# Kernel optimization log

Measured on AMD Instinct MI355X. Metric: run time of the kernel, lower is better.

## Reference

```python
import jax, jax.numpy as jnp
import numpy as np

LRELU_GAIN = 2.0 ** 0.5  # util.lrelu_gain (assumed sqrt(2))
EPS = 1e-8


def upsample2_bilinear_ac(x):
    # F.upsample_bilinear == bilinear with align_corners=True, scale 2
    B, C, H, W = x.shape
    def lerp_axis(t, n, axis):
        c = jnp.arange(2 * n, dtype=jnp.float32) * (n - 1) / (2 * n - 1)
        i0 = jnp.floor(c).astype(jnp.int32)
        i1 = jnp.minimum(i0 + 1, n - 1)
        f = c - i0.astype(jnp.float32)
        a = jnp.take(t, i0, axis=axis)
        b = jnp.take(t, i1, axis=axis)
        shape = [1] * t.ndim
        shape[axis] = 2 * n
        f = f.reshape(shape)
        return a * (1.0 - f) + b * f
    x = lerp_axis(x, H, 2)
    x = lerp_axis(x, W, 3)
    return x


def conv1x1(x, weight, bias, gain):
    # Conv2dNormalizedLR with kernel_size=1: he = gain/sqrt(in)
    cin = weight.shape[1]
    he = gain / float(cin) ** 0.5
    y = jnp.einsum('bihw,oi->bohw', x, weight[:, :, 0, 0] * he)
    return y + bias[None, :, None, None]


def mod_conv3x3(x, weight, style, gain):
    # weight: [Cin, Cout, 3, 3]; style: [B, Cin]
    cin, cout, k, _ = weight.shape
    he = gain / float(cin * k * k) ** 0.5
    wmod = style[:, :, None, None, None] * (weight * he)[None]  # [B,Cin,Cout,k,k]
    # demodulation: normalize over (in, kh, kw) per out channel
    d = jax.lax.rsqrt(jnp.sum(wmod * wmod, axis=(1, 3, 4), keepdims=True) + EPS)
    wmod = wmod * d
    # conv_transpose2d(stride=1, pad=1, k=3) == conv2d with transposed+flipped kernel, pad=1
    kern = jnp.flip(jnp.transpose(wmod, (0, 2, 1, 3, 4)), axis=(3, 4))  # [B,Cout,Cin,k,k]
    def one(xb, kb):
        return jax.lax.conv_general_dilated(
            xb[None], kb, (1, 1), ((1, 1), (1, 1)),
            dimension_numbers=('NCHW', 'OIHW', 'NCHW'))[0]
    y = jax.vmap(one)(x, kern)
    return y * gain


def noise_affine(noise, w_s, b_s, w_b, b_b):
    # Baff*: 1x1 conv from 1 channel, gain=1 -> he=1
    ys = noise * w_s[None, :, 0, None, 0, None][:, :, :, 0] if False else noise * w_s[:, 0, 0, 0][None, :, None, None] + b_s[None, :, None, None]
    yb = noise * w_b[:, 0, 0, 0][None, :, None, None] + b_b[None, :, None, None]
    return ys, yb


def block_forward(x, w, noise1, noise2, conv1_w, bias1, conv2_w, bias2,
                  Aaff1_w, Aaff1_b, Aaff2_w, Aaff2_b,
                  Baff1s_w, Baff1s_b, Baff1b_w, Baff1b_b,
                  Baff2s_w, Baff2s_b, Baff2b_w, Baff2b_b,
                  rgb_w, rgb_b):
    x = upsample2_bilinear_ac(x)
    style1 = conv1x1(w, Aaff1_w, Aaff1_b, 1.0)[:, :, 0, 0]  # [B, Cin]
    x = mod_conv3x3(x, conv1_w, style1, LRELU_GAIN)
    ys, yb = noise_affine(noise1, Baff1s_w, Baff1s_b, Baff1b_w, Baff1b_b)
    x = x * ys + yb + bias1
    x = jax.nn.leaky_relu(x, 0.2)
    style2 = conv1x1(w, Aaff2_w, Aaff2_b, 1.0)[:, :, 0, 0]
    x = mod_conv3x3(x, conv2_w, style2, LRELU_GAIN)
    ys, yb = noise_affine(noise2, Baff2s_w, Baff2s_b, Baff2b_w, Baff2b_b)
    x = x * ys + yb + bias2
    x = jax.nn.leaky_relu(x, 0.2)
    rgb = conv1x1(x, rgb_w, rgb_b, 0.03)
    return x, rgb


def setup_inputs() -> dict:
    key = jax.random.key(0)
    ks = jax.random.split(key, 20)
    B, Cin, Cout, Wd, H, W = 8, 512, 512, 512, 32, 32
    inp = {
        'x': jax.random.normal(ks[0], (B, Cin, H, W), jnp.float32),
        'w': jax.random.normal(ks[1], (B, Wd, 1, 1), jnp.float32),
        'noise1': jax.random.normal(ks[2], (B, 1, 2 * H, 2 * W), jnp.float32),
        'noise2': jax.random.normal(ks[3], (B, 1, 2 * H, 2 * W), jnp.float32),
        'conv1_w': jax.random.normal(ks[4], (Cin, Cout, 3, 3), jnp.float32),
        'bias1': jnp.zeros((1, Cout, 1, 1), jnp.float32),
        'conv2_w': jax.random.normal(ks[5], (Cout, Cout, 3, 3), jnp.float32),
        'bias2': jnp.zeros((1, Cout, 1, 1), jnp.float32),
        'Aaff1_w': jax.random.normal(ks[6], (Cin, Wd, 1, 1), jnp.float32),
        'Aaff1_b': jnp.zeros((Cin,), jnp.float32),
        'Aaff2_w': jax.random.normal(ks[7], (Cout, Wd, 1, 1), jnp.float32),
        'Aaff2_b': jnp.zeros((Cout,), jnp.float32),
        'Baff1s_w': jax.random.normal(ks[8], (Cout, 1, 1, 1), jnp.float32) * 0.1,
        'Baff1s_b': jnp.ones((Cout,), jnp.float32),
        'Baff1b_w': jax.random.normal(ks[9], (Cout, 1, 1, 1), jnp.float32) * 0.1,
        'Baff1b_b': jnp.zeros((Cout,), jnp.float32),
        'Baff2s_w': jax.random.normal(ks[10], (Cout, 1, 1, 1), jnp.float32) * 0.1,
        'Baff2s_b': jnp.ones((Cout,), jnp.float32),
        'Baff2b_w': jax.random.normal(ks[11], (Cout, 1, 1, 1), jnp.float32) * 0.1,
        'Baff2b_b': jnp.zeros((Cout,), jnp.float32),
        'rgb_w': jax.random.normal(ks[12], (3, Cout, 1, 1), jnp.float32),
        'rgb_b': jnp.zeros((3,), jnp.float32),
    }
    return inp


def reference(x, w, noise1, noise2, conv1_w, bias1, conv2_w, bias2,
              Aaff1_w, Aaff1_b, Aaff2_w, Aaff2_b,
              Baff1s_w, Baff1s_b, Baff1b_w, Baff1b_b,
              Baff2s_w, Baff2s_b, Baff2b_w, Baff2b_b,
              rgb_w, rgb_b):
    return block_forward(x, w, noise1, noise2, conv1_w, bias1, conv2_w, bias2,
                         Aaff1_w, Aaff1_b, Aaff2_w, Aaff2_b,
                         Baff1s_w, Baff1s_b, Baff1b_w, Baff1b_b,
                         Baff2s_w, Baff2s_b, Baff2b_w, Baff2b_b,
                         rgb_w, rgb_b)
```

## Files before the change

kernel.cpp:

```cpp
#include <hip/hip_runtime.h>
#include <hip/hip_bf16.h>

#define BB 8
#define CC 512
#define HO 64
#define HP 66
#define NPIX (BB*HO*HO)

typedef float f32x4 __attribute__((ext_vector_type(4)));
typedef __bf16 bf16x8 __attribute__((ext_vector_type(8)));
using bf16 = __hip_bfloat16;

__device__ __forceinline__ void gload16(const void* g, void* l) {
    __builtin_amdgcn_global_load_lds((const __attribute__((address_space(1))) void*)g,
                                     (__attribute__((address_space(3))) void*)l, 16, 0, 0);
}

__device__ __forceinline__ float waveRedSum(float v) {
    #pragma unroll
    for (int off = 32; off; off >>= 1) v += __shfl_down(v, off);
    return v;
}

__global__ void prep_weights(const float* __restrict__ Wsrc, float* __restrict__ S2ho,
                             bf16* __restrict__ keffT, float he) {
    int t = blockIdx.x * blockDim.x + threadIdx.x;
    int i = t & (CC-1), o = t >> 9;
    const float* wp = Wsrc + (i*CC + o)*9;
    float v[9]; float s2 = 0.f;
    #pragma unroll
    for (int k = 0; k < 9; ++k) { v[k] = wp[k] * he; s2 += v[k]*v[k]; }
    S2ho[o*CC + i] = s2;
    #pragma unroll
    for (int tp = 0; tp < 9; ++tp) keffT[(tp*CC + o)*CC + i] = (bf16)v[8 - tp];
}

__global__ void style_kernel(const float* __restrict__ w,
                             const float* __restrict__ A1, const float* __restrict__ A1b,
                             const float* __restrict__ A2, const float* __restrict__ A2b,
                             float* __restrict__ s1, float* __restrict__ s2) {
    int wid = (blockIdx.x * blockDim.x + threadIdx.x) >> 6;
    int lane = threadIdx.x & 63;
    int set = wid >= BB*CC; int rem = set ? wid - BB*CC : wid;
    int b = rem >> 9, i = rem & (CC-1);
    const float* A = set ? A2 : A1;
    const float* wb = w + b*CC;
    float sum = 0.f;
    for (int d = lane; d < CC; d += 64) sum += wb[d] * A[i*CC + d];
    sum = waveRedSum(sum);
    if (lane == 0) {
        float r = sum * 0.04419417382415922f + (set ? A2b : A1b)[i];
        (set ? s2 : s1)[b*CC + i] = r;
    }
}

__global__ void demod_kernel(const float* __restrict__ s1, const float* __restrict__ S21,
                             const float* __restrict__ s2, const float* __restrict__ S22,
                             float* __restrict__ dg1, float* __restrict__ dg2, float gain) {
    int wid = (blockIdx.x * blockDim.x + threadIdx.x) >> 6;
    int lane = threadIdx.x & 63;
    int set = wid >= BB*CC; int rem = set ? wid - BB*CC : wid;
    int b = rem >> 9, o = rem & (CC-1);
    const float* st = (set ? s2 : s1) + b*CC;
    const float* S2 = (set ? S22 : S21) + o*CC;
    float sum = 0.f;
    for (int i = lane; i < CC; i += 64) { float sv = st[i]; sum += sv*sv*S2[i]; }
    sum = waveRedSum(sum);
    if (lane == 0) (set ? dg2 : dg1)[b*CC + o] = gain * rsqrtf(sum + 1e-8f);
}

__global__ void upsample_mod(const float* __restrict__ x, const float* __restrict__ s1,
                             bf16* __restrict__ xs1) {
    __shared__ float usl[16][CC];
    int blk = blockIdx.x;
    int i = threadIdx.x;
    int b = blk >> 10, rem = blk & 1023, p = rem >> 4, q0 = (rem & 15) << 2;
    const float scale = 31.0f / 63.0f;
    float chf = p * scale; int h0 = (int)chf; float fh = chf - h0; int h1 = min(h0 + 1, 31);
    int wa = min(((int)(q0 * scale)) & ~3, 24);
    const float* xb = x + ((size_t)(b*CC + i) << 10);
    f32x4 r00 = *(const f32x4*)(xb + (h0 << 5) + wa);
    f32x4 r01 = *(const f32x4*)(xb + (h0 << 5) + wa + 4);
    f32x4 r10 = *(const f32x4*)(xb + (h1 << 5) + wa);
    f32x4 r11 = *(const f32x4*)(xb + (h1 << 5) + wa + 4);
    #pragma unroll
    for (int k = 0; k < 4; ++k) {
        usl[k][i] = r00[k]; usl[4 + k][i] = r01[k];
        usl[8 + k][i] = r10[k]; usl[12 + k][i] = r11[k];
    }
    float sv = s1[b*CC + i];
    #pragma unroll
    for (int dq = 0; dq < 4; ++dq) {
        int q = q0 + dq;
        float cwf = q * scale; int w0 = (int)cwf; float fw = cwf - w0;
        int i0 = w0 - wa, i1 = min(w0 + 1, 31) - wa;
        float v00 = usl[i0][i], v01 = usl[i1][i];
        float v10 = usl[8 + i0][i], v11 = usl[8 + i1][i];
        float va = v00*(1.f-fh) + v10*fh;
        float vb = v01*(1.f-fh) + v11*fh;
        float v  = (va*(1.f-fw) + vb*fw) * sv;
        xs1[(((b*HP) + p + 1)*HP + (q + 1))*CC + i] = (bf16)v;
    }
}

#define SB  __builtin_amdgcn_sched_barrier(0)
#define BAR __builtin_amdgcn_s_barrier()
#define VMC(n)  asm volatile("s_waitcnt vmcnt(" #n ")" ::: "memory")
#define LGKM(n) asm volatile("s_waitcnt lgkmcnt(" #n ")" ::: "memory")

#define STAGE_A(d, h, U) do { \
    gload16((U) + aThr + (h)*(HP*1024),                 ldsA + (d)*32768 + (h)*16384); \
    gload16((U) + aThr + (h)*(HP*1024) + 2*(HP*1024),   ldsA + (d)*32768 + (h)*16384 + 8192); \
} while (0)

#define STAGE_B(d, h, U) do { \
    gload16((U) + bThr + (h)*32768,                     ldsB + (d)*32768 + (h)*16384); \
    gload16((U) + bThr + (h)*32768 + 131072,            ldsB + (d)*32768 + (h)*16384 + 8192); \
} while (0)

#define LOAD_A(d, fh) do { \
    _Pragma("unroll") \
    for (int fmq = 0; fmq < 4; ++fmq) { \
        afr[fmq][0] = *(const bf16x8*)(aRd + (d)*32768 + (fh)*16384 + fmq*2048 + swz0); \
        afr[fmq][1] = *(const bf16x8*)(aRd + (d)*32768 + (fh)*16384 + fmq*2048 + swz1); \
    } } while (0)

#define LOAD_B(d, nh) do { \
    _Pragma("unroll") \
    for (int fnq = 0; fnq < 2; ++fnq) { \
        bfr[nh][fnq][0] = *(const bf16x8*)(bRd + (d)*32768 + (nh)*16384 + fnq*2048 + swz0); \
        bfr[nh][fnq][1] = *(const bf16x8*)(bRd + (d)*32768 + (nh)*16384 + fnq*2048 + swz1); \
    } } while (0)

#define QUAD(fh, nh) do { \
    __builtin_amdgcn_s_setprio(1); \
    _Pragma("unroll") \
    for (int kc = 0; kc < 2; ++kc) \
    { _Pragma("unroll") \
      for (int fmq = 0; fmq < 4; ++fmq) \
      { _Pragma("unroll") \
        for (int fnq = 0; fnq < 2; ++fnq) \
            acc[(fh)*4+fmq][(nh)*2+fnq] = __builtin_amdgcn_mfma_f32_16x16x32_bf16( \
                afr[fmq][kc], bfr[nh][fnq][kc], acc[(fh)*4+fmq][(nh)*2+fnq], 0, 0, 0); } } \
    __builtin_amdgcn_s_setprio(0); } while (0)

#define PHSTEP(cur, nxt, aN1, bN1, aN2, g1, g3) do { \
     \
    LOAD_A(cur, 0); \
    LOAD_B(cur, 0); \
    if (g1) STAGE_B(nxt, 0, bN1); \
    LGKM(8); SB; BAR; LGKM(0); SB; \
    QUAD(0, 0); \
    VMC(4); SB; BAR; SB; \
     \
    LOAD_B(cur, 1); \
    if (g1) STAGE_B(nxt, 1, bN1); \
    SB; BAR; LGKM(0); SB; \
    QUAD(0, 1); \
    SB; BAR; SB; \
     \
    LOAD_A(cur, 1); \
    if (g1) STAGE_A(nxt, 1, aN1); \
    SB; BAR; LGKM(0); SB; \
    QUAD(1, 1); \
    SB; BAR; SB; \
     \
    if (g3) STAGE_A(cur, 0, aN2); \
    SB; BAR; SB; \
    QUAD(1, 0); \
    if (g3) { VMC(6); } else { VMC(0); } \
    SB; BAR; SB; \
} while (0)

template<int PHASE>
__global__ __launch_bounds__(512, 2) void conv_gemm(
    const bf16* __restrict__ xs, const bf16* __restrict__ keffT,
    const float* __restrict__ dg, const float* __restrict__ noise,
    const float* __restrict__ nsw, const float* __restrict__ nsb,
    const float* __restrict__ nbw, const float* __restrict__ nbb,
    const float* __restrict__ biasv, const float* __restrict__ stnext,
    bf16* __restrict__ outb, float* __restrict__ outf) {
    __shared__ __attribute__((aligned(16))) bf16 As[32768];
    __shared__ __attribute__((aligned(16))) bf16 Bs[32768];
    const int tid = threadIdx.x;
    const int wave = tid >> 6, lane = tid & 63;
    const int tileId = ((blockIdx.x & 7) << 5) + (blockIdx.x >> 3);
    const int mtile = tileId >> 1, ntile = tileId & 1;
    const int m0 = mtile << 8, n0 = ntile << 8;
    const int b  = m0 >> 12;
    const int p0 = (m0 & 4095) >> 6;
    const int wm = wave >> 2, wn = wave & 3;
    const int l15 = lane & 15;

    const int srcSwz = (((tid & 7) ^ ((tid >> 3) & 7)) << 4);
    const int aThr = ((tid >> 3) << 10) + srcSwz;
    const int bThr = (((tid >> 8) & 1) << 16) + (((tid >> 3) & 31) << 10) + srcSwz;
    char* const ldsA = (char*)As + tid*16;
    char* const ldsB = (char*)Bs + tid*16;

    const char* const aRd = (const char*)As + (((wm << 6) + l15) << 7);
    const char* const bRd = (const char*)Bs + (((wn << 5) + l15) << 7);
    const int swz0 = (((lane >> 4)    ) ^ (lane & 7)) << 4;
    const int swz1 = (((lane >> 4) | 4) ^ (lane & 7)) << 4;

    f32x4 acc[8][4];
    #pragma unroll
    for (int i_ = 0; i_ < 8; ++i_)
        #pragma unroll
        for (int j_ = 0; j_ < 4; ++j_) acc[i_][j_] = f32x4{0.f, 0.f, 0.f, 0.f};
    bf16x8 afr[4][2], bfr[2][2][2];

    auto abase = [&](int st) -> const char* {
        int t = st >> 3; int dh = (t*11) >> 5; int dw = t - dh*3;
        return (const char*)xs + ((size_t)((b*HP + p0 + dh)*HP + dw) << 10) + ((st & 7) << 7);
    };
    auto bbase = [&](int st) -> const char* {
        int t = st >> 3;
        return (const char*)keffT + ((size_t)(t*CC + n0) << 10) + ((st & 7) << 7);
    };

    {
        const char* a0 = abase(0); const char* b0 = bbase(0); const char* a1 = abase(1);
        STAGE_A(0, 0, a0);
        STAGE_B(0, 0, b0);
        STAGE_B(0, 1, b0);
        STAGE_A(0, 1, a0);
        STAGE_A(1, 0, a1);
        VMC(6); SB; BAR; SB;
    }

    #pragma unroll 1
    for (int it = 0; it < 36; ++it) {
        const bool more = (it < 35);
        const char* aE = abase(2*it + 1); const char* bE = bbase(2*it + 1);
        const char* aO = abase(2*it + 2); const char* bO = bbase(2*it + 2);
        const char* aO2 = abase(2*it + 3);
        PHSTEP(0, 1, aE, bE, aO,  true, more);
        PHSTEP(1, 0, aO, bO, aO2, more, more);
    }

    const float* dgb = dg + b*CC;
    int nIdx[4]; float pdg[4], pnsw[4], pnsb[4], pnbw[4], pnbb[4], pbias[4], pst[4];
    #pragma unroll
    for (int fn = 0; fn < 4; ++fn) {
        int n = n0 + (wn << 6) + (fn << 4) + l15;
        nIdx[fn] = n;
        pdg[fn] = dgb[n]; pnsw[fn] = nsw[n]; pnsb[fn] = nsb[n];
        pnbw[fn] = nbw[n]; pnbb[fn] = nbb[n]; pbias[fn] = biasv[n];
        if (PHASE == 1) pst[fn] = stnext[b*CC + n]; else pst[fn] = 0.f;
    }
    #pragma unroll
    for (int fm = 0; fm < 8; ++fm) {
        #pragma unroll
        for (int r = 0; r < 4; ++r) {
            int mloc = m0 + (wm << 7) + (fm << 4) + ((lane >> 4) << 2) + r;
            float ns = noise[mloc];
            int prow = (mloc & 4095) >> 6, qcol = mloc & 63;
            #pragma unroll
            for (int fn = 0; fn < 4; ++fn) {
                float v = acc[fm][fn][r] * pdg[fn];
                v = v * (ns*pnsw[fn] + pnsb[fn]) + (ns*pnbw[fn] + pnbb[fn]) + pbias[fn];
                v = fmaxf(v, 0.2f*v);
                if (PHASE == 1) {
                    outb[(((b*HP) + prow + 1)*HP + (qcol + 1))*CC + nIdx[fn]] =
                        (bf16)(v * pst[fn]);
                } else {
                    outf[((b*CC + nIdx[fn]) << 12) + (mloc & 4095)] = v;
                }
            }
        }
    }
}

__global__ void rgb_kernel(const float* __restrict__ xf, const float* __restrict__ rgbw,
                           const float* __restrict__ rgbb, float* __restrict__ out) {
    __shared__ float red[3][4][64];
    int tid = threadIdx.x;
    int wv = tid >> 6, ln = tid & 63;
    int pix = blockIdx.x * 64 + ln;
    int b = pix >> 12, rem = pix & 4095;
    const float* xb = xf + (((size_t)b*CC) << 12) + rem;
    float a0 = 0.f, a1 = 0.f, a2 = 0.f;
    int o0 = wv << 7;
    #pragma unroll 8
    for (int o = o0; o < o0 + 128; ++o) {
        float xv = xb[(size_t)o << 12];
        a0 += xv * rgbw[o]; a1 += xv * rgbw[CC+o]; a2 += xv * rgbw[2*CC+o];
    }
    red[0][wv][ln] = a0; red[1][wv][ln] = a1; red[2][wv][ln] = a2;
    __syncthreads();
    if (wv == 0) {
        const float he = 0.03f * 0.04419417382415922f;
        #pragma unroll
        for (int c = 0; c < 3; ++c) {
            float s = red[c][0][ln] + red[c][1][ln] + red[c][2][ln] + red[c][3][ln];
            out[(b*3+c)*4096 + rem] = s*he + rgbb[c];
        }
    }
}

extern "C" void kernel_launch(void* const* d_in, const int* in_sizes, int n_in,
                              void* d_out, int out_size, void* d_ws, size_t ws_size,
                              hipStream_t stream) {
    const float* x      = (const float*)d_in[0];
    const float* w      = (const float*)d_in[1];
    const float* noise1 = (const float*)d_in[2];
    const float* noise2 = (const float*)d_in[3];
    const float* conv1w = (const float*)d_in[4];
    const float* bias1  = (const float*)d_in[5];
    const float* conv2w = (const float*)d_in[6];
    const float* bias2  = (const float*)d_in[7];
    const float* A1w = (const float*)d_in[8];
    const float* A1b = (const float*)d_in[9];
    const float* A2w = (const float*)d_in[10];
    const float* A2b = (const float*)d_in[11];
    const float* B1sw = (const float*)d_in[12];
    const float* B1sb = (const float*)d_in[13];
    const float* B1bw = (const float*)d_in[14];
    const float* B1bb = (const float*)d_in[15];
    const float* B2sw = (const float*)d_in[16];
    const float* B2sb = (const float*)d_in[17];
    const float* B2bw = (const float*)d_in[18];
    const float* B2bb = (const float*)d_in[19];
    const float* rgbw = (const float*)d_in[20];
    const float* rgbb = (const float*)d_in[21];

    char* ws = (char*)d_ws;
    size_t off = 0;
    auto alloc = [&](size_t bytes) { char* p = ws + off; off += (bytes + 255) & ~(size_t)255; return p; };
    const size_t xsBytes = (size_t)BB*HP*HP*CC*2;
    bf16* xs1 = (bf16*)alloc(xsBytes);
    bf16* xs2 = (bf16*)alloc(xsBytes);
    bf16* kT1 = (bf16*)alloc((size_t)9*CC*CC*2);
    bf16* kT2 = (bf16*)alloc((size_t)9*CC*CC*2);
    float* S21 = (float*)alloc((size_t)CC*CC*4);
    float* S22 = (float*)alloc((size_t)CC*CC*4);
    float* s1  = (float*)alloc(BB*CC*4);
    float* s2  = (float*)alloc(BB*CC*4);
    float* dg1 = (float*)alloc(BB*CC*4);
    float* dg2 = (float*)alloc(BB*CC*4);

    float* outx   = (float*)d_out;
    float* outrgb = outx + (size_t)BB*CC*HO*HO;

    hipMemsetAsync(xs1, 0, xsBytes, stream);
    hipMemsetAsync(xs2, 0, xsBytes, stream);

    const float gain = 1.41421356237309515f;
    const float he = gain / sqrtf(512.f * 9.f);
    prep_weights<<<CC*CC/256, 256, 0, stream>>>(conv1w, S21, kT1, he);
    prep_weights<<<CC*CC/256, 256, 0, stream>>>(conv2w, S22, kT2, he);
    style_kernel<<<2*BB*CC/4, 256, 0, stream>>>(w, A1w, A1b, A2w, A2b, s1, s2);
    demod_kernel<<<2*BB*CC/4, 256, 0, stream>>>(s1, S21, s2, S22, dg1, dg2, gain);
    upsample_mod<<<BB*HO*16, CC, 0, stream>>>(x, s1, xs1);
    conv_gemm<1><<<(NPIX/256)*(CC/256), 512, 0, stream>>>(
        xs1, kT1, dg1, noise1, B1sw, B1sb, B1bw, B1bb, bias1, s2, xs2, nullptr);
    conv_gemm<2><<<(NPIX/256)*(CC/256), 512, 0, stream>>>(
        xs2, kT2, dg2, noise2, B2sw, B2sb, B2bw, B2bb, bias2, nullptr, nullptr, outx);
    rgb_kernel<<<NPIX/64, 256, 0, stream>>>(outx, rgbw, rgbb, outrgb);
}
```

Before: 384.3 us.

## Switch conv GEMM to 32x32x16 MFMA and zero only halo borders

```diff
diff --git a/kernel.cpp b/kernel.cpp
--- a/kernel.cpp
+++ b/kernel.cpp
@@ -8,6 +8,7 @@
 #define NPIX (BB*HO*HO)
 
 typedef float f32x4 __attribute__((ext_vector_type(4)));
+typedef float f32x16 __attribute__((ext_vector_type(16)));
 typedef __bf16 bf16x8 __attribute__((ext_vector_type(8)));
 using bf16 = __hip_bfloat16;
 
@@ -103,6 +104,20 @@
     }
 }
 
+__global__ void halo_zero(bf16* __restrict__ xs1, bf16* __restrict__ xs2) {
+    int blk = blockIdx.x;
+    bf16* dst = (blk & 1) ? xs2 : xs1;
+    int idx = blk >> 1;
+    int b = idx / 260, rm = idx - b*260;
+    int p, q;
+    if (rm < 66)       { p = 0;        q = rm; }
+    else if (rm < 132) { p = 65;       q = rm - 66; }
+    else if (rm < 196) { p = rm - 131; q = 0; }
+    else               { p = rm - 195; q = 65; }
+    f32x4* d4 = (f32x4*)(dst + ((size_t)((b*HP + p)*HP + q)) * CC);
+    d4[threadIdx.x] = f32x4{0.f, 0.f, 0.f, 0.f};
+}
+
 #define SB  __builtin_amdgcn_sched_barrier(0)
 #define BAR __builtin_amdgcn_s_barrier()
 #define VMC(n)  asm volatile("s_waitcnt vmcnt(" #n ")" ::: "memory")
@@ -120,28 +135,26 @@
 
 #define LOAD_A(d, fh) do { \
     _Pragma("unroll") \
-    for (int fmq = 0; fmq < 4; ++fmq) { \
-        afr[fmq][0] = *(const bf16x8*)(aRd + (d)*32768 + (fh)*16384 + fmq*2048 + swz0); \
-        afr[fmq][1] = *(const bf16x8*)(aRd + (d)*32768 + (fh)*16384 + fmq*2048 + swz1); \
+    for (int tmh = 0; tmh < 2; ++tmh) { \
+        _Pragma("unroll") \
+        for (int kc = 0; kc < 4; ++kc) \
+            afr[tmh][kc] = *(const bf16x8*)(aRd + (d)*32768 + (fh)*16384 + tmh*4096 + swz[kc]); \
     } } while (0)
 
-#define LOAD_B(d, nh) do { \
+#define LOAD_B(d, tn) do { \
     _Pragma("unroll") \
-    for (int fnq = 0; fnq < 2; ++fnq) { \
-        bfr[nh][fnq][0] = *(const bf16x8*)(bRd + (d)*32768 + (nh)*16384 + fnq*2048 + swz0); \
-        bfr[nh][fnq][1] = *(const bf16x8*)(bRd + (d)*32768 + (nh)*16384 + fnq*2048 + swz1); \
-    } } while (0)
-
-#define QUAD(fh, nh) do { \
+    for (int kc = 0; kc < 4; ++kc) \
+        bfr[tn][kc] = *(const bf16x8*)(bRd + (d)*32768 + (tn)*16384 + swz[kc]); \
+    } while (0)
+
+#define QUAD(fh, tn) do { \
     __builtin_amdgcn_s_setprio(1); \
     _Pragma("unroll") \
-    for (int kc = 0; kc < 2; ++kc) \
+    for (int kc = 0; kc < 4; ++kc) \
     { _Pragma("unroll") \
-      for (int fmq = 0; fmq < 4; ++fmq) \
-      { _Pragma("unroll") \
-        for (int fnq = 0; fnq < 2; ++fnq) \
-            acc[(fh)*4+fmq][(nh)*2+fnq] = __builtin_amdgcn_mfma_f32_16x16x32_bf16( \
-                afr[fmq][kc], bfr[nh][fnq][kc], acc[(fh)*4+fmq][(nh)*2+fnq], 0, 0, 0); } } \
+      for (int tmh = 0; tmh < 2; ++tmh) \
+        acc[(fh)*2+tmh][tn] = __builtin_amdgcn_mfma_f32_32x32x16_bf16( \
+            afr[tmh][kc], bfr[tn][kc], acc[(fh)*2+tmh][tn], 0, 0, 0); } \
     __builtin_amdgcn_s_setprio(0); } while (0)
 
 #define PHSTEP(cur, nxt, aN1, bN1, aN2, g1, g3) do { \
@@ -173,7 +186,7 @@
 } while (0)
 
 template<int PHASE>
-__global__ __launch_bounds__(512, 2) void conv_gemm(
+__global__ __launch_bounds__(512, 1) void conv_gemm(
     const bf16* __restrict__ xs, const bf16* __restrict__ keffT,
     const float* __restrict__ dg, const float* __restrict__ noise,
     const float* __restrict__ nsw, const float* __restrict__ nsb,
@@ -190,7 +203,7 @@
     const int b  = m0 >> 12;
     const int p0 = (m0 & 4095) >> 6;
     const int wm = wave >> 2, wn = wave & 3;
-    const int l15 = lane & 15;
+    const int l31 = lane & 31;
 
     const int srcSwz = (((tid & 7) ^ ((tid >> 3) & 7)) << 4);
     const int aThr = ((tid >> 3) << 10) + srcSwz;
@@ -198,17 +211,21 @@
     char* const ldsA = (char*)As + tid*16;
     char* const ldsB = (char*)Bs + tid*16;
 
-    const char* const aRd = (const char*)As + (((wm << 6) + l15) << 7);
-    const char* const bRd = (const char*)Bs + (((wn << 5) + l15) << 7);
-    const int swz0 = (((lane >> 4)    ) ^ (lane & 7)) << 4;
-    const int swz1 = (((lane >> 4) | 4) ^ (lane & 7)) << 4;
-
-    f32x4 acc[8][4];
-    #pragma unroll
-    for (int i_ = 0; i_ < 8; ++i_)
+    const char* const aRd = (const char*)As + (wm << 13) + (l31 << 7);
+    const char* const bRd = (const char*)Bs + (((wn << 5) + l31) << 7);
+    int swz[4];
+    #pragma unroll
+    for (int kc = 0; kc < 4; ++kc)
+        swz[kc] = ((((kc << 1) | (lane >> 5)) ^ (lane & 7)) << 4);
+
+    f32x16 acc[4][2];
+    #pragma unroll
+    for (int i_ = 0; i_ < 4; ++i_)
         #pragma unroll
-        for (int j_ = 0; j_ < 4; ++j_) acc[i_][j_] = f32x4{0.f, 0.f, 0.f, 0.f};
-    bf16x8 afr[4][2], bfr[2][2][2];
+        for (int j_ = 0; j_ < 2; ++j_)
+            #pragma unroll
+            for (int e_ = 0; e_ < 16; ++e_) acc[i_][j_][e_] = 0.f;
+    bf16x8 afr[2][4], bfr[2][4];
 
     auto abase = [&](int st) -> const char* {
         int t = st >> 3; int dh = (t*11) >> 5; int dw = t - dh*3;
@@ -240,32 +257,36 @@
     }
 
     const float* dgb = dg + b*CC;
-    int nIdx[4]; float pdg[4], pnsw[4], pnsb[4], pnbw[4], pnbb[4], pbias[4], pst[4];
-    #pragma unroll
-    for (int fn = 0; fn < 4; ++fn) {
-        int n = n0 + (wn << 6) + (fn << 4) + l15;
-        nIdx[fn] = n;
-        pdg[fn] = dgb[n]; pnsw[fn] = nsw[n]; pnsb[fn] = nsb[n];
-        pnbw[fn] = nbw[n]; pnbb[fn] = nbb[n]; pbias[fn] = biasv[n];
-        if (PHASE == 1) pst[fn] = stnext[b*CC + n]; else pst[fn] = 0.f;
-    }
-    #pragma unroll
-    for (int fm = 0; fm < 8; ++fm) {
+    int nIdx[2]; float pdg[2], pnsw[2], pnsb[2], pnbw[2], pnbb[2], pbias[2], pst[2];
+    #pragma unroll
+    for (int tn = 0; tn < 2; ++tn) {
+        int n = n0 + (wn << 6) + (tn << 5) + l31;
+        nIdx[tn] = n;
+        pdg[tn] = dgb[n]; pnsw[tn] = nsw[n]; pnsb[tn] = nsb[n];
+        pnbw[tn] = nbw[n]; pnbb[tn] = nbb[n]; pbias[tn] = biasv[n];
+        if (PHASE == 1) pst[tn] = stnext[b*CC + n]; else pst[tn] = 0.f;
+    }
+    #pragma unroll
+    for (int tm = 0; tm < 4; ++tm) {
         #pragma unroll
-        for (int r = 0; r < 4; ++r) {
-            int mloc = m0 + (wm << 7) + (fm << 4) + ((lane >> 4) << 2) + r;
-            float ns = noise[mloc];
-            int prow = (mloc & 4095) >> 6, qcol = mloc & 63;
+        for (int rq = 0; rq < 4; ++rq) {
+            int mbase = m0 + (wm << 7) + (tm << 5) + (rq << 3) + ((lane >> 5) << 2);
             #pragma unroll
-            for (int fn = 0; fn < 4; ++fn) {
-                float v = acc[fm][fn][r] * pdg[fn];
-                v = v * (ns*pnsw[fn] + pnsb[fn]) + (ns*pnbw[fn] + pnbb[fn]) + pbias[fn];
-                v = fmaxf(v, 0.2f*v);
-                if (PHASE == 1) {
-                    outb[(((b*HP) + prow + 1)*HP + (qcol + 1))*CC + nIdx[fn]] =
-                        (bf16)(v * pst[fn]);
-                } else {
-                    outf[((b*CC + nIdx[fn]) << 12) + (mloc & 4095)] = v;
+            for (int rr = 0; rr < 4; ++rr) {
+                int mloc = mbase + rr;
+                float ns = noise[mloc];
+                int prow = (mloc & 4095) >> 6, qcol = mloc & 63;
+                #pragma unroll
+                for (int tn = 0; tn < 2; ++tn) {
+                    float v = acc[tm][tn][rq*4 + rr] * pdg[tn];
+                    v = v * (ns*pnsw[tn] + pnsb[tn]) + (ns*pnbw[tn] + pnbb[tn]) + pbias[tn];
+                    v = fmaxf(v, 0.2f*v);
+                    if (PHASE == 1) {
+                        outb[(((b*HP) + prow + 1)*HP + (qcol + 1))*CC + nIdx[tn]] =
+                            (bf16)(v * pst[tn]);
+                    } else {
+                        outf[((b*CC + nIdx[tn]) << 12) + (mloc & 4095)] = v;
+                    }
                 }
             }
         }
@@ -343,11 +364,9 @@
     float* outx   = (float*)d_out;
     float* outrgb = outx + (size_t)BB*CC*HO*HO;
 
-    hipMemsetAsync(xs1, 0, xsBytes, stream);
-    hipMemsetAsync(xs2, 0, xsBytes, stream);
-
     const float gain = 1.41421356237309515f;
     const float he = gain / sqrtf(512.f * 9.f);
+    halo_zero<<<4160, 64, 0, stream>>>(xs1, xs2);
     prep_weights<<<CC*CC/256, 256, 0, stream>>>(conv1w, S21, kT1, he);
     prep_weights<<<CC*CC/256, 256, 0, stream>>>(conv2w, S22, kT2, he);
     style_kernel<<<2*BB*CC/4, 256, 0, stream>>>(w, A1w, A1b, A2w, A2b, s1, s2);
```

Measured after the change: 420.6 us. 1.09x slower.
